# Kernel tuning notes

Hardware: AMD Instinct MI355X
Metric: run time of the kernel (lower is better)

Reference implementation:

```python
import jax, jax.numpy as jnp
import numpy as np

META_DIM, CIN, COUT, K = 32, 64, 64, 3
B, N, S = 32, 256, 64


def setup_inputs() -> dict:
    key = jax.random.key(0)
    k1, k2, k3, k4, k5, k6 = jax.random.split(key, 6)
    scale = 1.0 / np.sqrt(META_DIM)
    return {
        "meta_knowledge": jax.random.normal(k1, (B, N, META_DIM), dtype=jnp.float32),
        "x": jax.random.normal(k2, (B, N, S, CIN), dtype=jnp.float32),
        "w_lin_w": jax.random.normal(k3, (CIN * COUT * K, META_DIM), dtype=jnp.float32) * scale,
        "w_lin_b": jax.random.normal(k4, (CIN * COUT * K,), dtype=jnp.float32) * scale,
        "b_lin_w": jax.random.normal(k5, (COUT, META_DIM), dtype=jnp.float32) * scale,
        "b_lin_b": jax.random.normal(k6, (COUT,), dtype=jnp.float32) * scale,
    }


def reference(meta_knowledge, x, w_lin_w, w_lin_b, b_lin_w, b_lin_b):
    # meta_knowledge: [B, N, M]; x: [B, N, S, Cin]
    b, n, s, cin = x.shape
    cout = b_lin_w.shape[0]
    k = w_lin_w.shape[0] // (cin * cout)
    s_out = s - k + 1

    # Hypernetwork: per-(batch,node) conv weights and biases
    # w: [B, N, Cout, Cin, K]
    w = (jnp.einsum("bnm,pm->bnp", meta_knowledge, w_lin_w) + w_lin_b)
    w = w.reshape(b, n, cout, cin, k)
    # bias: [B, N, Cout]
    bias = jnp.einsum("bnm,om->bno", meta_knowledge, b_lin_w) + b_lin_b

    # Sliding windows over seq axis (valid conv): [B, N, S_out, K, Cin]
    x_win = jnp.stack([x[:, :, j : j + s_out, :] for j in range(k)], axis=3)

    # Per-group dynamic conv as batched contraction: [B, N, S_out, Cout]
    out = jnp.einsum("bntkc,bnock->bnto", x_win, w) + bias[:, :, None, :]
    return out
```

## Files before the change

### kernel.cpp

```cpp
#include <hip/hip_runtime.h>
#include <hip/hip_bf16.h>


#define BN_TOT   8192
#define C_IN     64
#define C_OUT    64
#define M_DIM    32
#define S_OUT    62

#define NT       8
#define NTHREADS 1024
#define XSTR     40
#define XNODE    (64 * XSTR)
#define XBUF     (NT * XNODE)
#define OSTR     104
#define WNODE    (16 * OSTR + 8)
#define WBUF     (NT * WNODE)
#define DYNSH    (2 * XBUF + 2 * WBUF)
#define DYNB     (DYNSH * 2)
#define WLW_ROWS 12288
#define WS_NEED  (WLW_ROWS * M_DIM * 2 + WLW_ROWS * 4)

typedef __attribute__((ext_vector_type(8))) short bf16x8;
typedef __attribute__((ext_vector_type(4))) float f32x4;

static __device__ __forceinline__ short f2bf(float f) {
    return __bfloat16_as_short(__float2bfloat16(f));
}

static __device__ __forceinline__ bf16x8 cvt8(float4 a, float4 b) {
    bf16x8 r;
    r[0] = f2bf(a.x); r[1] = f2bf(a.y); r[2] = f2bf(a.z); r[3] = f2bf(a.w);
    r[4] = f2bf(b.x); r[5] = f2bf(b.y); r[6] = f2bf(b.z); r[7] = f2bf(b.w);
    return r;
}

static __device__ __forceinline__ void barrier_lgkm() {
    asm volatile("s_waitcnt lgkmcnt(0)" ::: "memory");
    __builtin_amdgcn_s_barrier();
    asm volatile("" ::: "memory");
}

extern "C" __global__ void wlw_to_bf16(const float* __restrict__ src,
                                       short* __restrict__ dst) {
    const int i = (blockIdx.x * 256 + threadIdx.x) * 8;
    const float4 a = *reinterpret_cast<const float4*>(src + i);
    const float4 b = *reinterpret_cast<const float4*>(src + i + 4);
    *reinterpret_cast<bf16x8*>(dst + i) = cvt8(a, b);
}

extern "C" __global__ void wlb_rearr(const float* __restrict__ wlb,
                                     float* __restrict__ wlbR) {
    const int i = blockIdx.x * 256 + threadIdx.x;
    const int o = i / 192;
    const int r = i - o * 192;
    const int k = r >> 6;
    const int c = r & 63;
    wlbR[i] = wlb[o * 192 + c * 3 + k];
}

struct XReg { float4 a0, a1, b0, b1; };

template <int USE_WS>
__global__ void __launch_bounds__(NTHREADS, 4)
metaconv_fused(const float* __restrict__ meta,
               const float* __restrict__ x,
               const float* __restrict__ wlw,
               const short* __restrict__ wlwbf,
               const float* __restrict__ wlb,
               const float* __restrict__ wlbR,
               const float* __restrict__ blw,
               const float* __restrict__ blb,
               float* __restrict__ out)
{
    extern __shared__ __align__(16) short dynsm[];
    short* xbuf = dynsm;
    short* wbuf = dynsm + 2 * XBUF;
    __shared__ float bias_s[NT][C_OUT];

    const int tid   = threadIdx.x;
    const int wave  = tid >> 6;
    const int lane  = tid & 63;
    const int l16   = lane & 15;
    const int g     = lane >> 4;
    const int node  = wave & (NT - 1);
    const int thalf = wave >> 3;
    const int bn0   = blockIdx.x * NT;

    const float* xsrc = x + (size_t)(bn0 + node) * (64 * C_IN);
    const int ts0 = thalf * 32;
    const int row0 = ts0 + (lane >> 2), gr0 = lane & 3;
    const int row1 = ts0 + ((64 + lane) >> 2), gr1 = lane & 3;

    auto stage_load = [&](int c0, XReg& xr) {
        const float* p0 = xsrc + row0 * 64 + c0 + gr0 * 8;
        const float* p1 = xsrc + row1 * 64 + c0 + gr1 * 8;
        xr.a0 = *reinterpret_cast<const float4*>(p0);
        xr.a1 = *reinterpret_cast<const float4*>(p0 + 4);
        xr.b0 = *reinterpret_cast<const float4*>(p1);
        xr.b1 = *reinterpret_cast<const float4*>(p1 + 4);
    };
    auto stage_write = [&](int half, const XReg& xr) {
        short* xd = xbuf + half * XBUF + node * XNODE;
        *reinterpret_cast<bf16x8*>(xd + row0 * XSTR + gr0 * 8) = cvt8(xr.a0, xr.a1);
        *reinterpret_cast<bf16x8*>(xd + row1 * XSTR + gr1 * 8) = cvt8(xr.b0, xr.b1);
    };

    XReg xr0;
    stage_load(0, xr0);

    if (tid < NT * C_OUT) {
        const int bnode = tid >> 6;
        const int o     = tid & 63;
        const float* mrow = meta + (size_t)(bn0 + bnode) * M_DIM;
        const float* brow = blw + o * M_DIM;
        float s = blb[o];
        #pragma unroll
        for (int m = 0; m < M_DIM; ++m) s += mrow[m] * brow[m];
        bias_s[bnode][o] = s;
    }

    bf16x8 metaF;
    {
        const float* mp = meta + (size_t)(bn0 + (l16 & (NT - 1))) * M_DIM + g * 8;
        metaF = cvt8(*reinterpret_cast<const float4*>(mp),
                     *reinterpret_cast<const float4*>(mp + 4));
    }

    auto hyper = [&](int oq, int c0, int half) {
        const int og = oq * 16 + wave;
        short* wd = wbuf + half * WBUF;
        #pragma unroll
        for (int ch = 0; ch < 2; ++ch) {
            #pragma unroll
            for (int k = 0; k < 3; ++k) {
                const int pr = og * 192 + (c0 + ch * 16 + l16) * 3 + k;
                bf16x8 aF;
                f32x4 Cf;
                if constexpr (USE_WS) {
                    aF = *reinterpret_cast<const bf16x8*>(wlwbf + (size_t)pr * M_DIM + g * 8);
                    const float4 cf = *reinterpret_cast<const float4*>(
                        wlbR + (og * 3 + k) * 64 + c0 + ch * 16 + g * 4);
                    Cf[0] = cf.x; Cf[1] = cf.y; Cf[2] = cf.z; Cf[3] = cf.w;
                } else {
                    const float* wp = wlw + (size_t)pr * M_DIM + g * 8;
                    aF = cvt8(*reinterpret_cast<const float4*>(wp),
                              *reinterpret_cast<const float4*>(wp + 4));
                    const int cb = c0 + ch * 16 + g * 4;
                    const int pb = og * 192 + k;
                    Cf[0] = wlb[pb + (cb + 0) * 3];
                    Cf[1] = wlb[pb + (cb + 1) * 3];
                    Cf[2] = wlb[pb + (cb + 2) * 3];
                    Cf[3] = wlb[pb + (cb + 3) * 3];
                }
                const f32x4 d = __builtin_amdgcn_mfma_f32_16x16x32_bf16(aF, metaF, Cf, 0, 0, 0);
                if (l16 < NT) {
                    const int off = l16 * WNODE + wave * OSTR + k * 32 + ch * 16 + g * 4;
                    *reinterpret_cast<short4*>(&wd[off]) =
                        make_short4(f2bf(d[0]), f2bf(d[1]), f2bf(d[2]), f2bf(d[3]));
                }
            }
        }
    };

    const f32x4 ZV = {0.f, 0.f, 0.f, 0.f};
    f32x4 acc[2][4];
    #pragma unroll
    for (int t = 0; t < 2; ++t)
        #pragma unroll
        for (int o = 0; o < 4; ++o) acc[t][o] = ZV;

    auto conv = [&](int oq, int cc, int half) {
        const short* wn = wbuf + half * WBUF + node * WNODE;
        const short* xn = xbuf + cc * XBUF + node * XNODE;
        bf16x8 B[3];
        #pragma unroll
        for (int k = 0; k < 3; ++k)
            B[k] = *reinterpret_cast<const bf16x8*>(wn + l16 * OSTR + k * 32 + g * 8);
        #pragma unroll
        for (int ttl = 0; ttl < 2; ++ttl) {
            #pragma unroll
            for (int k = 0; k < 3; ++k) {
                int row = thalf * 32 + ttl * 16 + l16 + k;
                row = row < 63 ? row : 63;
                const bf16x8 A = *reinterpret_cast<const bf16x8*>(
                    xn + row * XSTR + g * 8);
                acc[ttl][oq] = __builtin_amdgcn_mfma_f32_16x16x32_bf16(
                    A, B[k], acc[ttl][oq], 0, 0, 0);
            }
        }
    };

    stage_write(0, xr0);
    hyper(0, 0, 0);
    barrier_lgkm();

    XReg xr1;
    #pragma unroll
    for (int cc = 0; cc < 2; ++cc) {
        #pragma unroll
        for (int oq = 0; oq < 4; ++oq) {
            const int P = cc * 4 + oq;
            if (P == 0) stage_load(32, xr1);
            if (P < 7) {
                const int Pn = P + 1;
                hyper(Pn & 3, (Pn >> 2) * 32, Pn & 1);
            }
            conv(oq, cc, P & 1);
            if (P == 3) stage_write(1, xr1);
            barrier_lgkm();
        }
    }

    float* ob = out + (size_t)(bn0 + node) * (S_OUT * C_OUT);
    #pragma unroll
    for (int ttl = 0; ttl < 2; ++ttl) {
        #pragma unroll
        for (int ot = 0; ot < 4; ++ot) {
            const int o  = ot * 16 + l16;
            const float bv = bias_s[node][o];
            #pragma unroll
            for (int r = 0; r < 4; ++r) {
                const int t = thalf * 32 + ttl * 16 + g * 4 + r;
                if (t < S_OUT) ob[t * C_OUT + o] = acc[ttl][ot][r] + bv;
            }
        }
    }
}

extern "C" void kernel_launch(void* const* d_in, const int* in_sizes, int n_in,
                              void* d_out, int out_size, void* d_ws, size_t ws_size,
                              hipStream_t stream) {
    const float* meta = (const float*)d_in[0];
    const float* x    = (const float*)d_in[1];
    const float* wlw  = (const float*)d_in[2];
    const float* wlb  = (const float*)d_in[3];
    const float* blw  = (const float*)d_in[4];
    const float* blb  = (const float*)d_in[5];
    float* out = (float*)d_out;
    (void)in_sizes; (void)n_in; (void)out_size;

    short* wlwbf = (short*)d_ws;
    float* wlbR  = (float*)((char*)d_ws + (size_t)WLW_ROWS * M_DIM * 2);

    if (ws_size >= (size_t)WS_NEED) {
        (void)hipFuncSetAttribute((const void*)&metaconv_fused<1>,
                                  hipFuncAttributeMaxDynamicSharedMemorySize, DYNB);
        wlw_to_bf16<<<dim3(WLW_ROWS * M_DIM / (256 * 8)), dim3(256), 0, stream>>>(wlw, wlwbf);
        wlb_rearr<<<dim3(WLW_ROWS / 256), dim3(256), 0, stream>>>(wlb, wlbR);
        metaconv_fused<1><<<dim3(BN_TOT / NT), dim3(NTHREADS), DYNB, stream>>>(
            meta, x, wlw, wlwbf, wlb, wlbR, blw, blb, out);
    } else {
        (void)hipFuncSetAttribute((const void*)&metaconv_fused<0>,
                                  hipFuncAttributeMaxDynamicSharedMemorySize, DYNB);
        metaconv_fused<0><<<dim3(BN_TOT / NT), dim3(NTHREADS), DYNB, stream>>>(
            meta, x, wlw, wlwbf, wlb, wlbR, blw, blb, out);
    }
}
```

Baseline: 142.9 us.

## Load conv input fragments directly from global into registers, drop LDS staging

Removes the shared-memory staging buffer for x. Each wave now loads its MFMA A-fragments (including the three overlapping shifted windows) straight from global memory, converts them to bf16 and keeps them in registers across all output quarters. This saves LDS capacity, LDS writes and reads, and the custom barrier, and may allow more blocks per CU. In exchange each x row is read up to three times from global or cache, register pressure rises, and the second-half load now sits right before use with less latency hiding.

```diff
diff --git a/kernel.cpp b/kernel.cpp
--- a/kernel.cpp
+++ b/kernel.cpp
@@ -10,14 +10,9 @@
 
 #define NT       8
 #define NTHREADS 1024
-#define XSTR     40
-#define XNODE    (64 * XSTR)
-#define XBUF     (NT * XNODE)
 #define OSTR     104
 #define WNODE    (16 * OSTR + 8)
 #define WBUF     (NT * WNODE)
-#define DYNSH    (2 * XBUF + 2 * WBUF)
-#define DYNB     (DYNSH * 2)
 #define WLW_ROWS 12288
 #define WS_NEED  (WLW_ROWS * M_DIM * 2 + WLW_ROWS * 4)
 
@@ -33,12 +28,6 @@
     r[0] = f2bf(a.x); r[1] = f2bf(a.y); r[2] = f2bf(a.z); r[3] = f2bf(a.w);
     r[4] = f2bf(b.x); r[5] = f2bf(b.y); r[6] = f2bf(b.z); r[7] = f2bf(b.w);
     return r;
-}
-
-static __device__ __forceinline__ void barrier_lgkm() {
-    asm volatile("s_waitcnt lgkmcnt(0)" ::: "memory");
-    __builtin_amdgcn_s_barrier();
-    asm volatile("" ::: "memory");
 }
 
 extern "C" __global__ void wlw_to_bf16(const float* __restrict__ src,
@@ -58,8 +47,6 @@
     const int c = r & 63;
     wlbR[i] = wlb[o * 192 + c * 3 + k];
 }
-
-struct XReg { float4 a0, a1, b0, b1; };
 
 template <int USE_WS>
 __global__ void __launch_bounds__(NTHREADS, 4)
@@ -73,9 +60,7 @@
                const float* __restrict__ blb,
                float* __restrict__ out)
 {
-    extern __shared__ __align__(16) short dynsm[];
-    short* xbuf = dynsm;
-    short* wbuf = dynsm + 2 * XBUF;
+    __shared__ short wsh[2 * WBUF];
     __shared__ float bias_s[NT][C_OUT];
 
     const int tid   = threadIdx.x;
@@ -88,26 +73,6 @@
     const int bn0   = blockIdx.x * NT;
 
     const float* xsrc = x + (size_t)(bn0 + node) * (64 * C_IN);
-    const int ts0 = thalf * 32;
-    const int row0 = ts0 + (lane >> 2), gr0 = lane & 3;
-    const int row1 = ts0 + ((64 + lane) >> 2), gr1 = lane & 3;
-
-    auto stage_load = [&](int c0, XReg& xr) {
-        const float* p0 = xsrc + row0 * 64 + c0 + gr0 * 8;
-        const float* p1 = xsrc + row1 * 64 + c0 + gr1 * 8;
-        xr.a0 = *reinterpret_cast<const float4*>(p0);
-        xr.a1 = *reinterpret_cast<const float4*>(p0 + 4);
-        xr.b0 = *reinterpret_cast<const float4*>(p1);
-        xr.b1 = *reinterpret_cast<const float4*>(p1 + 4);
-    };
-    auto stage_write = [&](int half, const XReg& xr) {
-        short* xd = xbuf + half * XBUF + node * XNODE;
-        *reinterpret_cast<bf16x8*>(xd + row0 * XSTR + gr0 * 8) = cvt8(xr.a0, xr.a1);
-        *reinterpret_cast<bf16x8*>(xd + row1 * XSTR + gr1 * 8) = cvt8(xr.b0, xr.b1);
-    };
-
-    XReg xr0;
-    stage_load(0, xr0);
 
     if (tid < NT * C_OUT) {
         const int bnode = tid >> 6;
@@ -127,9 +92,27 @@
                      *reinterpret_cast<const float4*>(mp + 4));
     }
 
-    auto hyper = [&](int oq, int c0, int half) {
+    bf16x8 Abf[2][3];
+    auto load_A = [&](int c0) {
+        #pragma unroll
+        for (int ttl = 0; ttl < 2; ++ttl) {
+            float4 ra[3], rb[3];
+            #pragma unroll
+            for (int k = 0; k < 3; ++k) {
+                int row = thalf * 32 + ttl * 16 + l16 + k;
+                row = row < 63 ? row : 63;
+                const float* p = xsrc + row * 64 + c0 + g * 8;
+                ra[k] = *reinterpret_cast<const float4*>(p);
+                rb[k] = *reinterpret_cast<const float4*>(p + 4);
+            }
+            #pragma unroll
+            for (int k = 0; k < 3; ++k) Abf[ttl][k] = cvt8(ra[k], rb[k]);
+        }
+    };
+
+    auto hyper = [&](int c0, int oq, int buf) {
         const int og = oq * 16 + wave;
-        short* wd = wbuf + half * WBUF;
+        short* wd = wsh + buf * WBUF;
         #pragma unroll
         for (int ch = 0; ch < 2; ++ch) {
             #pragma unroll
@@ -170,45 +153,32 @@
         #pragma unroll
         for (int o = 0; o < 4; ++o) acc[t][o] = ZV;
 
-    auto conv = [&](int oq, int cc, int half) {
-        const short* wn = wbuf + half * WBUF + node * WNODE;
-        const short* xn = xbuf + cc * XBUF + node * XNODE;
-        bf16x8 B[3];
-        #pragma unroll
-        for (int k = 0; k < 3; ++k)
-            B[k] = *reinterpret_cast<const bf16x8*>(wn + l16 * OSTR + k * 32 + g * 8);
-        #pragma unroll
-        for (int ttl = 0; ttl < 2; ++ttl) {
-            #pragma unroll
-            for (int k = 0; k < 3; ++k) {
-                int row = thalf * 32 + ttl * 16 + l16 + k;
-                row = row < 63 ? row : 63;
-                const bf16x8 A = *reinterpret_cast<const bf16x8*>(
-                    xn + row * XSTR + g * 8);
-                acc[ttl][oq] = __builtin_amdgcn_mfma_f32_16x16x32_bf16(
-                    A, B[k], acc[ttl][oq], 0, 0, 0);
-            }
-        }
-    };
-
-    stage_write(0, xr0);
+    load_A(0);
     hyper(0, 0, 0);
-    barrier_lgkm();
-
-    XReg xr1;
+    __syncthreads();
+
     #pragma unroll
     for (int cc = 0; cc < 2; ++cc) {
         #pragma unroll
         for (int oq = 0; oq < 4; ++oq) {
             const int P = cc * 4 + oq;
-            if (P == 0) stage_load(32, xr1);
+            if (P == 4) load_A(32);
             if (P < 7) {
                 const int Pn = P + 1;
-                hyper(Pn & 3, (Pn >> 2) * 32, Pn & 1);
-            }
-            conv(oq, cc, P & 1);
-            if (P == 3) stage_write(1, xr1);
-            barrier_lgkm();
+                hyper((Pn >> 2) * 32, Pn & 3, Pn & 1);
+            }
+            const short* wn = wsh + (P & 1) * WBUF + node * WNODE;
+            bf16x8 B[3];
+            #pragma unroll
+            for (int k = 0; k < 3; ++k)
+                B[k] = *reinterpret_cast<const bf16x8*>(wn + l16 * OSTR + k * 32 + g * 8);
+            #pragma unroll
+            for (int ttl = 0; ttl < 2; ++ttl)
+                #pragma unroll
+                for (int k = 0; k < 3; ++k)
+                    acc[ttl][oq] = __builtin_amdgcn_mfma_f32_16x16x32_bf16(
+                        Abf[ttl][k], B[k], acc[ttl][oq], 0, 0, 0);
+            __syncthreads();
         }
     }
 
@@ -244,16 +214,12 @@
     float* wlbR  = (float*)((char*)d_ws + (size_t)WLW_ROWS * M_DIM * 2);
 
     if (ws_size >= (size_t)WS_NEED) {
-        (void)hipFuncSetAttribute((const void*)&metaconv_fused<1>,
-                                  hipFuncAttributeMaxDynamicSharedMemorySize, DYNB);
         wlw_to_bf16<<<dim3(WLW_ROWS * M_DIM / (256 * 8)), dim3(256), 0, stream>>>(wlw, wlwbf);
         wlb_rearr<<<dim3(WLW_ROWS / 256), dim3(256), 0, stream>>>(wlb, wlbR);
-        metaconv_fused<1><<<dim3(BN_TOT / NT), dim3(NTHREADS), DYNB, stream>>>(
+        metaconv_fused<1><<<dim3(BN_TOT / NT), dim3(NTHREADS), 0, stream>>>(
             meta, x, wlw, wlwbf, wlb, wlbR, blw, blb, out);
     } else {
-        (void)hipFuncSetAttribute((const void*)&metaconv_fused<0>,
-                                  hipFuncAttributeMaxDynamicSharedMemorySize, DYNB);
-        metaconv_fused<0><<<dim3(BN_TOT / NT), dim3(NTHREADS), DYNB, stream>>>(
+        metaconv_fused<0><<<dim3(BN_TOT / NT), dim3(NTHREADS), 0, stream>>>(
             meta, x, wlw, wlwbf, wlb, wlbR, blw, blb, out);
     }
 }
```

After: 165.7 us. +16.0%, slower.
